# Kernel tuning notes

Hardware: AMD Instinct MI355X
Metric: run time of the kernel (lower is better)

The kernel has to match this reference:

```python
import jax, jax.numpy as jnp
import numpy as np

S, N, H = 4096, 32, 512

def setup_inputs() -> dict:
    key = jax.random.key(0)
    ks = jax.random.split(key, 8)
    scale = 1.0 / np.sqrt(H)
    return {
        "hidden": jax.random.normal(ks[0], (N, H), dtype=jnp.float32),
        "encoder_outputs": jax.random.normal(ks[1], (S, N, H), dtype=jnp.float32),
        "W_w": jax.random.uniform(ks[2], (H, H), jnp.float32, -scale, scale),
        "W_b": jax.random.uniform(ks[3], (H,), jnp.float32, -scale, scale),
        "U_w": jax.random.uniform(ks[4], (H, H), jnp.float32, -scale, scale),
        "U_b": jax.random.uniform(ks[5], (H,), jnp.float32, -scale, scale),
        "v_w": jax.random.uniform(ks[6], (1, H), jnp.float32, -scale, scale),
        "v_b": jax.random.uniform(ks[7], (1,), jnp.float32, -scale, scale),
    }

def reference(hidden, encoder_outputs, W_w, W_b, U_w, U_b, v_w, v_b):
    # W(hidden): [N,H] -> broadcast over seq dim (equivalent to expand then Linear)
    wh = hidden @ W_w.T + W_b                      # [N, H]
    ue = jnp.einsum('snh,kh->snk', encoder_outputs, U_w) + U_b  # [S, N, H]
    energy = jnp.tanh(wh[None, :, :] + ue)         # [S, N, H]
    score = jnp.einsum('snh,oh->sno', energy, v_w) + v_b        # [S, N, 1]
    attention_weights = jax.nn.softmax(score, axis=0)           # softmax over seq
    context = jnp.sum(attention_weights * encoder_outputs, axis=0)  # [N, H]
    return (context, attention_weights)
```

## Files before the change

kernel.cpp:

```cpp
#include <hip/hip_runtime.h>
#include <hip/hip_bf16.h>

#define Sdim 4096
#define Ndim 32
#define Hdim 512
#define Mdim (Sdim * 32)

typedef __bf16 bf16x8 __attribute__((ext_vector_type(8)));
typedef float f32x4 __attribute__((ext_vector_type(4)));

__device__ __forceinline__ void load_lds16(const void* g, void* l) {
    __builtin_amdgcn_global_load_lds(
        (const __attribute__((address_space(1))) void*)g,
        (__attribute__((address_space(3))) void*)l, 16, 0, 0);
}

__device__ __forceinline__ float ftanh(float x) {
    float e = __expf(2.f * x);
    return 1.f - 2.f / (e + 1.f);
}

__global__ __launch_bounds__(256) void k_prep_bias(
    const float* __restrict__ hidden, const float* __restrict__ Ww,
    const float* __restrict__ Wb, const float* __restrict__ Ubias,
    float* __restrict__ bias_t) {
    const int t = threadIdx.x, w = t >> 6, lane = t & 63;
    const int cc = blockIdx.x * 4 + w;
    const float4 w0 = *(const float4*)(Ww + (size_t)cc * Hdim + lane * 8);
    const float4 w1 = *(const float4*)(Ww + (size_t)cc * Hdim + lane * 8 + 4);
    const float wb = Wb[cc] + Ubias[cc];
    for (int n = 0; n < Ndim; ++n) {
        const float4 h0 = *(const float4*)(hidden + n * Hdim + lane * 8);
        const float4 h1 = *(const float4*)(hidden + n * Hdim + lane * 8 + 4);
        float p = w0.x * h0.x + w0.y * h0.y + w0.z * h0.z + w0.w * h0.w +
                  w1.x * h1.x + w1.y * h1.y + w1.z * h1.z + w1.w * h1.w;
        p += __shfl_xor(p, 1);  p += __shfl_xor(p, 2);
        p += __shfl_xor(p, 4);  p += __shfl_xor(p, 8);
        p += __shfl_xor(p, 16); p += __shfl_xor(p, 32);
        if (lane == 0) bias_t[cc * Ndim + n] = p + wb;
    }
}

__global__ __launch_bounds__(256) void k_cvt(
    const float* __restrict__ src, unsigned short* __restrict__ dst) {
    const int i = blockIdx.x * 256 + threadIdx.x;
    float4 v = ((const float4*)src)[i];
    union { __hip_bfloat162 h[2]; ushort4 u; } r;
    r.h[0] = __float22bfloat162_rn(make_float2(v.x, v.y));
    r.h[1] = __float22bfloat162_rn(make_float2(v.z, v.w));
    ((ushort4*)dst)[i] = r.u;
}

__global__ __launch_bounds__(256, 3) void k_gemm_score(
    const float* __restrict__ enc,
    const unsigned short* __restrict__ Ub,
    const float* __restrict__ bias_t,
    const float* __restrict__ vw,
    float* __restrict__ scorep) {
    __shared__ __align__(16) unsigned short Asm[64 * 72];
    __shared__ __align__(16) unsigned short Bsm[256 * 64];
    __shared__ float ssm[4][64];

    const int t = threadIdx.x;
    const int lane = t & 63;
    const int w = t >> 6;
    const int c = lane & 15;
    const int q = lane >> 4;

    const int rowblk = blockIdx.x >> 1;
    const int colblk = blockIdx.x & 1;
    const int mBase = rowblk * 64;
    const int colBase = colblk * 256;

    const int ar = t >> 2;
    const int aq = t & 3;
    const float* aptr = enc + (size_t)(mBase + ar) * Hdim + aq * 16;
    unsigned short* awr = &Asm[ar * 72 + aq * 16];

    const int brow = lane >> 3;
    const int gchunk = (lane & 7) ^ (brow & 7);
    const unsigned short* bptr[8];
    unsigned short* bdst[8];
#pragma unroll
    for (int j = 0; j < 8; ++j) {
        const int r0 = w * 64 + j * 8;
        bptr[j] = Ub + (size_t)(colBase + r0 + brow) * Hdim + gchunk * 8;
        bdst[j] = &Bsm[r0 * 64];
    }

    f32x4 acc[4][4];
#pragma unroll
    for (int i = 0; i < 4; ++i)
#pragma unroll
        for (int j = 0; j < 4; ++j) acc[i][j] = (f32x4){0.f, 0.f, 0.f, 0.f};

    float4 pa0 = *(const float4*)(aptr + 0);
    float4 pa1 = *(const float4*)(aptr + 4);
    float4 pa2 = *(const float4*)(aptr + 8);
    float4 pa3 = *(const float4*)(aptr + 12);

#pragma unroll
    for (int kk = 0; kk < 8; ++kk) {
        __syncthreads();
        union { __hip_bfloat162 h[4]; bf16x8 v; } p0, p1;
        p0.h[0] = __float22bfloat162_rn(make_float2(pa0.x, pa0.y));
        p0.h[1] = __float22bfloat162_rn(make_float2(pa0.z, pa0.w));
        p0.h[2] = __float22bfloat162_rn(make_float2(pa1.x, pa1.y));
        p0.h[3] = __float22bfloat162_rn(make_float2(pa1.z, pa1.w));
        p1.h[0] = __float22bfloat162_rn(make_float2(pa2.x, pa2.y));
        p1.h[1] = __float22bfloat162_rn(make_float2(pa2.z, pa2.w));
        p1.h[2] = __float22bfloat162_rn(make_float2(pa3.x, pa3.y));
        p1.h[3] = __float22bfloat162_rn(make_float2(pa3.z, pa3.w));
        *(bf16x8*)(awr) = p0.v;
        *(bf16x8*)(awr + 8) = p1.v;
#pragma unroll
        for (int j = 0; j < 8; ++j)
            load_lds16(bptr[j] + kk * 64, bdst[j]);
        __syncthreads();
        if (kk < 7) {
            pa0 = *(const float4*)(aptr + (kk + 1) * 64);
            pa1 = *(const float4*)(aptr + (kk + 1) * 64 + 4);
            pa2 = *(const float4*)(aptr + (kk + 1) * 64 + 8);
            pa3 = *(const float4*)(aptr + (kk + 1) * 64 + 12);
        }
#pragma unroll
        for (int kh = 0; kh < 2; ++kh) {
            bf16x8 af[4], bfr[4];
#pragma unroll
            for (int mi = 0; mi < 4; ++mi)
                af[mi] = *(const bf16x8*)&Asm[(mi * 16 + c) * 72 + kh * 32 + q * 8];
#pragma unroll
            for (int ni = 0; ni < 4; ++ni) {
                const int r = w * 64 + ni * 16 + c;
                const int slot = (kh * 4 + q) ^ (c & 7);
                bfr[ni] = *(const bf16x8*)&Bsm[r * 64 + slot * 8];
            }
#pragma unroll
            for (int mi = 0; mi < 4; ++mi)
#pragma unroll
                for (int ni = 0; ni < 4; ++ni)
                    acc[mi][ni] = __builtin_amdgcn_mfma_f32_16x16x32_bf16(
                        af[mi], bfr[ni], acc[mi][ni], 0, 0, 0);
        }
    }

    float vcol[4];
#pragma unroll
    for (int ni = 0; ni < 4; ++ni)
        vcol[ni] = vw[colBase + w * 64 + ni * 16 + c];

#pragma unroll
    for (int mi = 0; mi < 4; ++mi) {
#pragma unroll
        for (int reg = 0; reg < 4; ++reg) {
            const int rl = mi * 16 + q * 4 + reg;
            const int n = rl & 31;
            float p = 0.f;
#pragma unroll
            for (int ni = 0; ni < 4; ++ni) {
                const int col = colBase + w * 64 + ni * 16 + c;
                float e = acc[mi][ni][reg] + bias_t[col * Ndim + n];
                p += vcol[ni] * ftanh(e);
            }
            p += __shfl_xor(p, 1);
            p += __shfl_xor(p, 2);
            p += __shfl_xor(p, 4);
            p += __shfl_xor(p, 8);
            if (c == 0) ssm[w][rl] = p;
        }
    }
    __syncthreads();
    if (t < 64) {
        const int m = mBase + t;
        const float s = ssm[0][t] + ssm[1][t] + ssm[2][t] + ssm[3][t];
        scorep[colblk * Mdim + (m & 31) * Sdim + (m >> 5)] = s;
    }
}

__global__ __launch_bounds__(256) void k_softmax(
    const float* __restrict__ scorep,
    float* __restrict__ wts) {
    const int n = blockIdx.x;
    const int t = threadIdx.x;
    const int w = t >> 6;
    __shared__ float row[Sdim];
    __shared__ float red[8];
    const float4* s0 = (const float4*)(scorep + n * Sdim);
    const float4* s1 = (const float4*)(scorep + Mdim + n * Sdim);

    float mx = -1e30f;
    for (int i = t; i < Sdim / 4; i += 256) {
        float4 a = s0[i], b = s1[i];
        float4 v;
        v.x = a.x + b.x; v.y = a.y + b.y; v.z = a.z + b.z; v.w = a.w + b.w;
        ((float4*)row)[i] = v;
        mx = fmaxf(mx, fmaxf(fmaxf(v.x, v.y), fmaxf(v.z, v.w)));
    }
#pragma unroll
    for (int o = 32; o > 0; o >>= 1) mx = fmaxf(mx, __shfl_xor(mx, o));
    if ((t & 63) == 0) red[w] = mx;
    __syncthreads();
    mx = fmaxf(fmaxf(red[0], red[1]), fmaxf(red[2], red[3]));

    float sum = 0.f;
    for (int i = t; i < Sdim; i += 256) sum += __expf(row[i] - mx);
#pragma unroll
    for (int o = 32; o > 0; o >>= 1) sum += __shfl_xor(sum, o);
    if ((t & 63) == 0) red[4 + w] = sum;
    __syncthreads();
    sum = red[4] + red[5] + red[6] + red[7];
    const float inv = 1.f / sum;
    for (int i = t; i < Sdim; i += 256)
        wts[n * Sdim + i] = __expf(row[i] - mx) * inv;
}

__global__ __launch_bounds__(256) void k_transpose(
    const float* __restrict__ wts, float* __restrict__ out_w) {
    __shared__ float tl[Ndim][129];
    const int s0 = blockIdx.x * 128;
    const int t = threadIdx.x;
    const int rr = t >> 3, cb = (t & 7) * 4;
#pragma unroll
    for (int j = 0; j < 4; ++j)
        *(float4*)&tl[rr][cb + j * 32] =
            *(const float4*)(wts + (size_t)rr * Sdim + s0 + cb + j * 32);
    __syncthreads();
    const int sl = t >> 1, nb = (t & 1) * 16;
#pragma unroll
    for (int j = 0; j < 4; ++j) {
        const int n0 = nb + j * 4;
        float4 v;
        v.x = tl[n0][sl]; v.y = tl[n0 + 1][sl];
        v.z = tl[n0 + 2][sl]; v.w = tl[n0 + 3][sl];
        *(float4*)(out_w + (size_t)(s0 + sl) * Ndim + n0) = v;
    }
}

__global__ __launch_bounds__(256) void k_context(
    const float* __restrict__ enc, const float* __restrict__ wts,
    float* __restrict__ part) {
    const int n = blockIdx.x & 31;
    const int sc = blockIdx.x >> 5;
    const int s0 = sc * 128;
    const int t = threadIdx.x;
    const int hv = t & 127;
    const int sl = t >> 7;
    const float* wrow = wts + (size_t)n * Sdim + s0;
    float4 a0 = {0, 0, 0, 0}, a1 = {0, 0, 0, 0};
    float4 a2 = {0, 0, 0, 0}, a3 = {0, 0, 0, 0};
    for (int i = sl * 4; i < 128; i += 8) {
        const float w0 = wrow[i], w1 = wrow[i + 1];
        const float w2 = wrow[i + 2], w3 = wrow[i + 3];
        const float4 e0 = *(const float4*)(enc + ((size_t)(s0 + i) * Ndim + n) * Hdim + hv * 4);
        const float4 e1 = *(const float4*)(enc + ((size_t)(s0 + i + 1) * Ndim + n) * Hdim + hv * 4);
        const float4 e2 = *(const float4*)(enc + ((size_t)(s0 + i + 2) * Ndim + n) * Hdim + hv * 4);
        const float4 e3 = *(const float4*)(enc + ((size_t)(s0 + i + 3) * Ndim + n) * Hdim + hv * 4);
        a0.x += w0 * e0.x; a0.y += w0 * e0.y; a0.z += w0 * e0.z; a0.w += w0 * e0.w;
        a1.x += w1 * e1.x; a1.y += w1 * e1.y; a1.z += w1 * e1.z; a1.w += w1 * e1.w;
        a2.x += w2 * e2.x; a2.y += w2 * e2.y; a2.z += w2 * e2.z; a2.w += w2 * e2.w;
        a3.x += w3 * e3.x; a3.y += w3 * e3.y; a3.z += w3 * e3.z; a3.w += w3 * e3.w;
    }
    a0.x += a1.x + a2.x + a3.x; a0.y += a1.y + a2.y + a3.y;
    a0.z += a1.z + a2.z + a3.z; a0.w += a1.w + a2.w + a3.w;
    __shared__ float4 red[128];
    if (sl == 1) red[hv] = a0;
    __syncthreads();
    if (sl == 0) {
        const float4 b = red[hv];
        float4 r;
        r.x = a0.x + b.x; r.y = a0.y + b.y; r.z = a0.z + b.z; r.w = a0.w + b.w;
        *(float4*)(part + (size_t)(sc * 32 + n) * Hdim + hv * 4) = r;
    }
}

__global__ __launch_bounds__(256) void k_ctx_reduce(
    const float* __restrict__ part, float* __restrict__ out) {
    const int j = blockIdx.x * 256 + threadIdx.x;
    float4 s = {0, 0, 0, 0};
    for (int i = 0; i < 32; ++i) {
        const float4 v = ((const float4*)part)[i * 4096 + j];
        s.x += v.x; s.y += v.y; s.z += v.z; s.w += v.w;
    }
    ((float4*)out)[j] = s;
}

extern "C" void kernel_launch(void* const* d_in, const int* in_sizes, int n_in,
                              void* d_out, int out_size, void* d_ws,
                              size_t ws_size, hipStream_t stream) {
    const float* hidden = (const float*)d_in[0];
    const float* enc    = (const float*)d_in[1];
    const float* Ww     = (const float*)d_in[2];
    const float* Wb     = (const float*)d_in[3];
    const float* Uw     = (const float*)d_in[4];
    const float* Ubias  = (const float*)d_in[5];
    const float* vw     = (const float*)d_in[6];

    float* out = (float*)d_out;

    char* ws = (char*)d_ws;
    float* wts           = (float*)(ws);
    unsigned short* Ub16 = (unsigned short*)(ws + (512 << 10));
    float* scorep        = (float*)(ws + (1024 << 10));
    float* bias_t        = (float*)(ws + (2048 << 10));
    float* part          = (float*)(ws + (512 << 10));

    k_prep_bias<<<128, 256, 0, stream>>>(hidden, Ww, Wb, Ubias, bias_t);
    k_cvt<<<256, 256, 0, stream>>>(Uw, Ub16);
    k_gemm_score<<<(Mdim / 64) * 2, 256, 0, stream>>>(enc, Ub16, bias_t, vw,
                                                      scorep);
    k_softmax<<<Ndim, 256, 0, stream>>>(scorep, wts);
    k_transpose<<<Sdim / 128, 256, 0, stream>>>(wts, out + Ndim * Hdim);
    k_context<<<Ndim * (Sdim / 128), 256, 0, stream>>>(enc, wts, part);
    k_ctx_reduce<<<16, 256, 0, stream>>>(part, out);
}
```

Measured before the change: 593.6 us.

## Pre-convert encoder outputs to bf16 and use 128x256 tile GEMM with async LDS loads

Adds a separate pass that converts the fp32 encoder outputs to bf16 in workspace. The score GEMM then uses direct global-to-LDS loads for both operands and a larger 128-row tile with 512 threads, so each block reuses the U tile across more rows. The extra pass writes 128 MB and reads 256 MB, and the GEMM then rereads the 128 MB bf16 copy, adding traffic in exchange for simpler GEMM loads and better reuse. A fallback to the old kernel is kept for when the workspace is too small.

Result: slower. 655.0 us (+10.4%).

```diff
diff --git a/kernel.cpp b/kernel.cpp
--- a/kernel.cpp
+++ b/kernel.cpp
@@ -8,6 +8,7 @@
 
 typedef __bf16 bf16x8 __attribute__((ext_vector_type(8)));
 typedef float f32x4 __attribute__((ext_vector_type(4)));
+typedef unsigned short ushort8v __attribute__((ext_vector_type(8)));
 
 __device__ __forceinline__ void load_lds16(const void* g, void* l) {
     __builtin_amdgcn_global_load_lds(
@@ -51,32 +52,147 @@
     ((ushort4*)dst)[i] = r.u;
 }
 
-__global__ __launch_bounds__(256, 3) void k_gemm_score(
-    const float* __restrict__ enc,
+__global__ __launch_bounds__(256) void k_cvt_enc(
+    const float* __restrict__ src, unsigned short* __restrict__ dst) {
+    const size_t i = (size_t)blockIdx.x * 256 + threadIdx.x;
+    const float4 a = ((const float4*)src)[2 * i];
+    const float4 b = ((const float4*)src)[2 * i + 1];
+    union { __hip_bfloat162 h[4]; ushort8v v; } r;
+    r.h[0] = __float22bfloat162_rn(make_float2(a.x, a.y));
+    r.h[1] = __float22bfloat162_rn(make_float2(a.z, a.w));
+    r.h[2] = __float22bfloat162_rn(make_float2(b.x, b.y));
+    r.h[3] = __float22bfloat162_rn(make_float2(b.z, b.w));
+    ((ushort8v*)dst)[i] = r.v;
+}
+
+__global__ __launch_bounds__(512, 3) void k_gemm_score(
+    const unsigned short* __restrict__ encb,
     const unsigned short* __restrict__ Ub,
     const float* __restrict__ bias_t,
     const float* __restrict__ vw,
     float* __restrict__ scorep) {
+    __shared__ __align__(16) unsigned short Asm[128 * 64];
+    __shared__ __align__(16) unsigned short Bsm[256 * 64];
+    __shared__ float ssm[4][128];
+
+    const int t = threadIdx.x;
+    const int lane = t & 63;
+    const int w = t >> 6;
+    const int wM = w >> 2;
+    const int wN = w & 3;
+    const int c = lane & 15;
+    const int q = lane >> 4;
+
+    const int rowblk = blockIdx.x >> 1;
+    const int colblk = blockIdx.x & 1;
+    const int mBase = rowblk * 128;
+    const int colBase = colblk * 256;
+
+    const int l3 = lane >> 3;
+    const int gch = (lane & 7) ^ (l3 & 7);
+    const unsigned short* aSrc[2];
+    unsigned short* aDst[2];
+#pragma unroll
+    for (int i = 0; i < 2; ++i) {
+        const int j = 2 * w + i;
+        aSrc[i] = encb + (size_t)(mBase + j * 8 + l3) * Hdim + gch * 8;
+        aDst[i] = &Asm[j * 8 * 64];
+    }
+    const unsigned short* bSrc[4];
+    unsigned short* bDst[4];
+#pragma unroll
+    for (int i = 0; i < 4; ++i) {
+        const int j = 4 * w + i;
+        bSrc[i] = Ub + (size_t)(colBase + j * 8 + l3) * Hdim + gch * 8;
+        bDst[i] = &Bsm[j * 8 * 64];
+    }
+
+    f32x4 acc[4][4];
+#pragma unroll
+    for (int i = 0; i < 4; ++i)
+#pragma unroll
+        for (int j = 0; j < 4; ++j) acc[i][j] = (f32x4){0.f, 0.f, 0.f, 0.f};
+
+#pragma unroll
+    for (int kk = 0; kk < 8; ++kk) {
+        __syncthreads();
+        load_lds16(aSrc[0] + kk * 64, aDst[0]);
+        load_lds16(aSrc[1] + kk * 64, aDst[1]);
+#pragma unroll
+        for (int i = 0; i < 4; ++i)
+            load_lds16(bSrc[i] + kk * 64, bDst[i]);
+        __syncthreads();
+
+#pragma unroll
+        for (int kh = 0; kh < 2; ++kh) {
+            bf16x8 af[4], bfr[4];
+            const int slot = (kh * 4 + q) ^ (c & 7);
+#pragma unroll
+            for (int mi = 0; mi < 4; ++mi) {
+                const int r = wM * 64 + mi * 16 + c;
+                af[mi] = *(const bf16x8*)&Asm[r * 64 + slot * 8];
+            }
+#pragma unroll
+            for (int ni = 0; ni < 4; ++ni) {
+                const int r = wN * 64 + ni * 16 + c;
+                bfr[ni] = *(const bf16x8*)&Bsm[r * 64 + slot * 8];
+            }
+#pragma unroll
+            for (int mi = 0; mi < 4; ++mi)
+#pragma unroll
+                for (int ni = 0; ni < 4; ++ni)
+                    acc[mi][ni] = __builtin_amdgcn_mfma_f32_16x16x32_bf16(
+                        af[mi], bfr[ni], acc[mi][ni], 0, 0, 0);
+        }
+    }
+
+    float vcol[4];
+#pragma unroll
+    for (int ni = 0; ni < 4; ++ni)
+        vcol[ni] = vw[colBase + wN * 64 + ni * 16 + c];
+
+#pragma unroll
+    for (int mi = 0; mi < 4; ++mi) {
+#pragma unroll
+        for (int reg = 0; reg < 4; ++reg) {
+            const int rl = wM * 64 + mi * 16 + q * 4 + reg;
+            const int n = rl & 31;
+            float p = 0.f;
+#pragma unroll
+            for (int ni = 0; ni < 4; ++ni) {
+                const int col = colBase + wN * 64 + ni * 16 + c;
+                float e = acc[mi][ni][reg] + bias_t[col * Ndim + n];
+                p += vcol[ni] * ftanh(e);
+            }
+            p += __shfl_xor(p, 1);
+            p += __shfl_xor(p, 2);
+            p += __shfl_xor(p, 4);
+            p += __shfl_xor(p, 8);
+            if (c == 0) ssm[wN][rl] = p;
+        }
+    }
+    __syncthreads();
+    if (t < 128) {
+        const int m = mBase + t;
+        const float s = ssm[0][t] + ssm[1][t] + ssm[2][t] + ssm[3][t];
+        scorep[colblk * Mdim + (m & 31) * Sdim + (m >> 5)] = s;
+    }
+}
+
+__global__ __launch_bounds__(256, 3) void k_gemm_score_fb(
+    const float* __restrict__ enc, const unsigned short* __restrict__ Ub,
+    const float* __restrict__ bias_t, const float* __restrict__ vw,
+    float* __restrict__ scorep) {
     __shared__ __align__(16) unsigned short Asm[64 * 72];
     __shared__ __align__(16) unsigned short Bsm[256 * 64];
     __shared__ float ssm[4][64];
-
-    const int t = threadIdx.x;
-    const int lane = t & 63;
-    const int w = t >> 6;
-    const int c = lane & 15;
-    const int q = lane >> 4;
-
-    const int rowblk = blockIdx.x >> 1;
-    const int colblk = blockIdx.x & 1;
-    const int mBase = rowblk * 64;
-    const int colBase = colblk * 256;
-
-    const int ar = t >> 2;
-    const int aq = t & 3;
+    const int t = threadIdx.x, lane = t & 63, w = t >> 6;
+    const int c = lane & 15, q = lane >> 4;
+    const int rowblk = blockIdx.x >> 1, colblk = blockIdx.x & 1;
+    const int mBase = rowblk * 64, colBase = colblk * 256;
+    const int ar = t >> 2, aq = t & 3;
     const float* aptr = enc + (size_t)(mBase + ar) * Hdim + aq * 16;
     unsigned short* awr = &Asm[ar * 72 + aq * 16];
-
     const int brow = lane >> 3;
     const int gchunk = (lane & 7) ^ (brow & 7);
     const unsigned short* bptr[8];
@@ -87,18 +203,13 @@
         bptr[j] = Ub + (size_t)(colBase + r0 + brow) * Hdim + gchunk * 8;
         bdst[j] = &Bsm[r0 * 64];
     }
-
     f32x4 acc[4][4];
 #pragma unroll
     for (int i = 0; i < 4; ++i)
 #pragma unroll
         for (int j = 0; j < 4; ++j) acc[i][j] = (f32x4){0.f, 0.f, 0.f, 0.f};
-
-    float4 pa0 = *(const float4*)(aptr + 0);
-    float4 pa1 = *(const float4*)(aptr + 4);
-    float4 pa2 = *(const float4*)(aptr + 8);
-    float4 pa3 = *(const float4*)(aptr + 12);
-
+    float4 pa0 = *(const float4*)(aptr + 0), pa1 = *(const float4*)(aptr + 4);
+    float4 pa2 = *(const float4*)(aptr + 8), pa3 = *(const float4*)(aptr + 12);
 #pragma unroll
     for (int kk = 0; kk < 8; ++kk) {
         __syncthreads();
@@ -114,8 +225,7 @@
         *(bf16x8*)(awr) = p0.v;
         *(bf16x8*)(awr + 8) = p1.v;
 #pragma unroll
-        for (int j = 0; j < 8; ++j)
-            load_lds16(bptr[j] + kk * 64, bdst[j]);
+        for (int j = 0; j < 8; ++j) load_lds16(bptr[j] + kk * 64, bdst[j]);
         __syncthreads();
         if (kk < 7) {
             pa0 = *(const float4*)(aptr + (kk + 1) * 64);
@@ -143,12 +253,9 @@
                         af[mi], bfr[ni], acc[mi][ni], 0, 0, 0);
         }
     }
-
     float vcol[4];
 #pragma unroll
-    for (int ni = 0; ni < 4; ++ni)
-        vcol[ni] = vw[colBase + w * 64 + ni * 16 + c];
-
+    for (int ni = 0; ni < 4; ++ni) vcol[ni] = vw[colBase + w * 64 + ni * 16 + c];
 #pragma unroll
     for (int mi = 0; mi < 4; ++mi) {
 #pragma unroll
@@ -178,8 +285,7 @@
 }
 
 __global__ __launch_bounds__(256) void k_softmax(
-    const float* __restrict__ scorep,
-    float* __restrict__ wts) {
+    const float* __restrict__ scorep, float* __restrict__ wts) {
     const int n = blockIdx.x;
     const int t = threadIdx.x;
     const int w = t >> 6;
@@ -187,7 +293,6 @@
     __shared__ float red[8];
     const float4* s0 = (const float4*)(scorep + n * Sdim);
     const float4* s1 = (const float4*)(scorep + Mdim + n * Sdim);
-
     float mx = -1e30f;
     for (int i = t; i < Sdim / 4; i += 256) {
         float4 a = s0[i], b = s1[i];
@@ -201,7 +306,6 @@
     if ((t & 63) == 0) red[w] = mx;
     __syncthreads();
     mx = fmaxf(fmaxf(red[0], red[1]), fmaxf(red[2], red[3]));
-
     float sum = 0.f;
     for (int i = t; i < Sdim; i += 256) sum += __expf(row[i] - mx);
 #pragma unroll
@@ -298,16 +402,24 @@
     float* out = (float*)d_out;
 
     char* ws = (char*)d_ws;
-    float* wts           = (float*)(ws);
-    unsigned short* Ub16 = (unsigned short*)(ws + (512 << 10));
-    float* scorep        = (float*)(ws + (1024 << 10));
-    float* bias_t        = (float*)(ws + (2048 << 10));
-    float* part          = (float*)(ws + (512 << 10));
+    unsigned short* Ub16 = (unsigned short*)(ws);
+    float* bias_t        = (float*)(ws + (512 << 10));
+    float* scorep        = (float*)(ws + (576 << 10));
+    float* wts           = (float*)(ws + (1600 << 10));
+    float* part          = (float*)(ws + (2112 << 10));
+    unsigned short* encb = (unsigned short*)(ws + (8 << 20));
+    const size_t REQ = (8ull << 20) + (size_t)Mdim * Hdim * 2;
 
     k_prep_bias<<<128, 256, 0, stream>>>(hidden, Ww, Wb, Ubias, bias_t);
     k_cvt<<<256, 256, 0, stream>>>(Uw, Ub16);
-    k_gemm_score<<<(Mdim / 64) * 2, 256, 0, stream>>>(enc, Ub16, bias_t, vw,
-                                                      scorep);
+    if (ws_size >= REQ) {
+        k_cvt_enc<<<32768, 256, 0, stream>>>(enc, encb);
+        k_gemm_score<<<(Mdim / 128) * 2, 512, 0, stream>>>(encb, Ub16, bias_t,
+                                                           vw, scorep);
+    } else {
+        k_gemm_score_fb<<<(Mdim / 64) * 2, 256, 0, stream>>>(enc, Ub16, bias_t,
+                                                             vw, scorep);
+    }
     k_softmax<<<Ndim, 256, 0, stream>>>(scorep, wts);
     k_transpose<<<Sdim / 128, 256, 0, stream>>>(wts, out + Ndim * Hdim);
     k_context<<<Ndim * (Sdim / 128), 256, 0, stream>>>(enc, wts, part);
```

## Pre-convert encoder to bf16 and keep U strip resident in LDS for GEMM

Applied to the files above, without the earlier changes.

A separate kernel now converts encoder_outputs to bf16 once. The score GEMM is restructured into persistent 512-thread blocks: each block holds a full 128-column strip of U in 128KB of dynamic LDS and loops over four row tiles, loading A fragments straight from global memory into registers with register double-buffering. The bias prep and U conversion kernels are merged into one launch, and the transpose kernel is folded into softmax as strided stores, which also now sums four partial scores. This aims to cut redundant fp32 encoder reads and per-tile LDS staging of U, at the cost of an extra full conversion pass over the encoder and uncoalesced weight-output writes.

Result: slower. 650.0 us (+9.5%).

```diff
diff --git a/kernel.cpp b/kernel.cpp
--- a/kernel.cpp
+++ b/kernel.cpp
@@ -8,6 +8,7 @@
 
 typedef __bf16 bf16x8 __attribute__((ext_vector_type(8)));
 typedef float f32x4 __attribute__((ext_vector_type(4)));
+typedef unsigned short ushort8v __attribute__((ext_vector_type(8)));
 
 __device__ __forceinline__ void load_lds16(const void* g, void* l) {
     __builtin_amdgcn_global_load_lds(
@@ -20,166 +21,175 @@
     return 1.f - 2.f / (e + 1.f);
 }
 
-__global__ __launch_bounds__(256) void k_prep_bias(
+__global__ __launch_bounds__(256) void k_prep(
     const float* __restrict__ hidden, const float* __restrict__ Ww,
     const float* __restrict__ Wb, const float* __restrict__ Ubias,
-    float* __restrict__ bias_t) {
-    const int t = threadIdx.x, w = t >> 6, lane = t & 63;
-    const int cc = blockIdx.x * 4 + w;
-    const float4 w0 = *(const float4*)(Ww + (size_t)cc * Hdim + lane * 8);
-    const float4 w1 = *(const float4*)(Ww + (size_t)cc * Hdim + lane * 8 + 4);
-    const float wb = Wb[cc] + Ubias[cc];
-    for (int n = 0; n < Ndim; ++n) {
-        const float4 h0 = *(const float4*)(hidden + n * Hdim + lane * 8);
-        const float4 h1 = *(const float4*)(hidden + n * Hdim + lane * 8 + 4);
-        float p = w0.x * h0.x + w0.y * h0.y + w0.z * h0.z + w0.w * h0.w +
-                  w1.x * h1.x + w1.y * h1.y + w1.z * h1.z + w1.w * h1.w;
-        p += __shfl_xor(p, 1);  p += __shfl_xor(p, 2);
-        p += __shfl_xor(p, 4);  p += __shfl_xor(p, 8);
-        p += __shfl_xor(p, 16); p += __shfl_xor(p, 32);
-        if (lane == 0) bias_t[cc * Ndim + n] = p + wb;
-    }
-}
-
-__global__ __launch_bounds__(256) void k_cvt(
+    const float* __restrict__ Uw, float* __restrict__ bias_t,
+    unsigned short* __restrict__ Ub16) {
+    if (blockIdx.x < 128) {
+        const int t = threadIdx.x, w = t >> 6, lane = t & 63;
+        const int cc = blockIdx.x * 4 + w;
+        const float4 w0 = *(const float4*)(Ww + (size_t)cc * Hdim + lane * 8);
+        const float4 w1 = *(const float4*)(Ww + (size_t)cc * Hdim + lane * 8 + 4);
+        const float wb = Wb[cc] + Ubias[cc];
+        for (int n = 0; n < Ndim; ++n) {
+            const float4 h0 = *(const float4*)(hidden + n * Hdim + lane * 8);
+            const float4 h1 = *(const float4*)(hidden + n * Hdim + lane * 8 + 4);
+            float p = w0.x * h0.x + w0.y * h0.y + w0.z * h0.z + w0.w * h0.w +
+                      w1.x * h1.x + w1.y * h1.y + w1.z * h1.z + w1.w * h1.w;
+            p += __shfl_xor(p, 1);  p += __shfl_xor(p, 2);
+            p += __shfl_xor(p, 4);  p += __shfl_xor(p, 8);
+            p += __shfl_xor(p, 16); p += __shfl_xor(p, 32);
+            if (lane == 0) bias_t[cc * Ndim + n] = p + wb;
+        }
+    } else {
+        const int i = (blockIdx.x - 128) * 256 + threadIdx.x;
+        float4 v = ((const float4*)Uw)[i];
+        union { __hip_bfloat162 h[2]; ushort4 u; } r;
+        r.h[0] = __float22bfloat162_rn(make_float2(v.x, v.y));
+        r.h[1] = __float22bfloat162_rn(make_float2(v.z, v.w));
+        ((ushort4*)Ub16)[i] = r.u;
+    }
+}
+
+__global__ __launch_bounds__(256) void k_cvt_enc(
     const float* __restrict__ src, unsigned short* __restrict__ dst) {
-    const int i = blockIdx.x * 256 + threadIdx.x;
-    float4 v = ((const float4*)src)[i];
-    union { __hip_bfloat162 h[2]; ushort4 u; } r;
-    r.h[0] = __float22bfloat162_rn(make_float2(v.x, v.y));
-    r.h[1] = __float22bfloat162_rn(make_float2(v.z, v.w));
-    ((ushort4*)dst)[i] = r.u;
-}
-
-__global__ __launch_bounds__(256, 3) void k_gemm_score(
-    const float* __restrict__ enc,
+    const size_t i = (size_t)blockIdx.x * 256 + threadIdx.x;
+    const float4 a = ((const float4*)src)[2 * i];
+    const float4 b = ((const float4*)src)[2 * i + 1];
+    union { __hip_bfloat162 h[4]; ushort8v v; } r;
+    r.h[0] = __float22bfloat162_rn(make_float2(a.x, a.y));
+    r.h[1] = __float22bfloat162_rn(make_float2(a.z, a.w));
+    r.h[2] = __float22bfloat162_rn(make_float2(b.x, b.y));
+    r.h[3] = __float22bfloat162_rn(make_float2(b.z, b.w));
+    ((ushort8v*)dst)[i] = r.v;
+}
+
+__global__ __launch_bounds__(512, 2) void k_gemm_score(
+    const unsigned short* __restrict__ encb,
     const unsigned short* __restrict__ Ub,
     const float* __restrict__ bias_t,
     const float* __restrict__ vw,
     float* __restrict__ scorep) {
-    __shared__ __align__(16) unsigned short Asm[64 * 72];
-    __shared__ __align__(16) unsigned short Bsm[256 * 64];
-    __shared__ float ssm[4][64];
+    extern __shared__ __align__(16) unsigned short Bsm[];
+    __shared__ float ssm[2][256];
 
     const int t = threadIdx.x;
     const int lane = t & 63;
     const int w = t >> 6;
+    const int wM = w >> 1;
+    const int wN = w & 1;
     const int c = lane & 15;
     const int q = lane >> 4;
 
-    const int rowblk = blockIdx.x >> 1;
-    const int colblk = blockIdx.x & 1;
-    const int mBase = rowblk * 64;
-    const int colBase = colblk * 256;
-
-    const int ar = t >> 2;
-    const int aq = t & 3;
-    const float* aptr = enc + (size_t)(mBase + ar) * Hdim + aq * 16;
-    unsigned short* awr = &Asm[ar * 72 + aq * 16];
-
-    const int brow = lane >> 3;
-    const int gchunk = (lane & 7) ^ (brow & 7);
-    const unsigned short* bptr[8];
-    unsigned short* bdst[8];
-#pragma unroll
-    for (int j = 0; j < 8; ++j) {
-        const int r0 = w * 64 + j * 8;
-        bptr[j] = Ub + (size_t)(colBase + r0 + brow) * Hdim + gchunk * 8;
-        bdst[j] = &Bsm[r0 * 64];
-    }
-
-    f32x4 acc[4][4];
-#pragma unroll
-    for (int i = 0; i < 4; ++i)
-#pragma unroll
-        for (int j = 0; j < 4; ++j) acc[i][j] = (f32x4){0.f, 0.f, 0.f, 0.f};
-
-    float4 pa0 = *(const float4*)(aptr + 0);
-    float4 pa1 = *(const float4*)(aptr + 4);
-    float4 pa2 = *(const float4*)(aptr + 8);
-    float4 pa3 = *(const float4*)(aptr + 12);
-
-#pragma unroll
-    for (int kk = 0; kk < 8; ++kk) {
+    const int strip = blockIdx.x & 3;
+    const int bgroup = blockIdx.x >> 2;
+    const int colBase = strip * 128;
+
+#pragma unroll
+    for (int j = 0; j < 16; ++j) {
+        const int col = w * 16 + j;
+        const unsigned short* src =
+            Ub + (size_t)(colBase + col) * Hdim + (lane ^ (col & 7)) * 8;
+        load_lds16(src, &Bsm[col * Hdim]);
+    }
+
+    float vcol[4];
+#pragma unroll
+    for (int ni = 0; ni < 4; ++ni)
+        vcol[ni] = vw[colBase + wN * 64 + ni * 16 + c];
+
+    __syncthreads();
+
+    for (int p = 0; p < 4; ++p) {
+        const int rowBase = (bgroup + p * 128) * 256;
+        const unsigned short* aRow[4];
+#pragma unroll
+        for (int mi = 0; mi < 4; ++mi)
+            aRow[mi] =
+                encb + (size_t)(rowBase + wM * 64 + mi * 16 + c) * Hdim + q * 8;
+
+        f32x4 acc[4][4];
+#pragma unroll
+        for (int i = 0; i < 4; ++i)
+#pragma unroll
+            for (int j = 0; j < 4; ++j) acc[i][j] = (f32x4){0.f, 0.f, 0.f, 0.f};
+
+        bf16x8 aC[4][2];
+#pragma unroll
+        for (int mi = 0; mi < 4; ++mi)
+#pragma unroll
+            for (int kh = 0; kh < 2; ++kh)
+                aC[mi][kh] = *(const bf16x8*)(aRow[mi] + kh * 32);
+
+#pragma unroll
+        for (int kk = 0; kk < 8; ++kk) {
+            bf16x8 aN[4][2];
+            if (kk < 7) {
+#pragma unroll
+                for (int mi = 0; mi < 4; ++mi)
+#pragma unroll
+                    for (int kh = 0; kh < 2; ++kh)
+                        aN[mi][kh] = *(const bf16x8*)(aRow[mi] +
+                                                      (kk + 1) * 64 + kh * 32);
+            }
+#pragma unroll
+            for (int kh = 0; kh < 2; ++kh) {
+                bf16x8 bfr[4];
+#pragma unroll
+                for (int ni = 0; ni < 4; ++ni) {
+                    const int col = wN * 64 + ni * 16 + c;
+                    const int slot = kk * 8 + ((kh * 4 + q) ^ (col & 7));
+                    bfr[ni] = *(const bf16x8*)&Bsm[col * Hdim + slot * 8];
+                }
+#pragma unroll
+                for (int mi = 0; mi < 4; ++mi)
+#pragma unroll
+                    for (int ni = 0; ni < 4; ++ni)
+                        acc[mi][ni] = __builtin_amdgcn_mfma_f32_16x16x32_bf16(
+                            aC[mi][kh], bfr[ni], acc[mi][ni], 0, 0, 0);
+            }
+            if (kk < 7) {
+#pragma unroll
+                for (int mi = 0; mi < 4; ++mi)
+#pragma unroll
+                    for (int kh = 0; kh < 2; ++kh) aC[mi][kh] = aN[mi][kh];
+            }
+        }
+
+#pragma unroll
+        for (int mi = 0; mi < 4; ++mi) {
+#pragma unroll
+            for (int reg = 0; reg < 4; ++reg) {
+                const int rl = wM * 64 + mi * 16 + q * 4 + reg;
+                const int n = rl & 31;
+                float psum = 0.f;
+#pragma unroll
+                for (int ni = 0; ni < 4; ++ni) {
+                    const int gcol = colBase + wN * 64 + ni * 16 + c;
+                    float e = acc[mi][ni][reg] + bias_t[gcol * Ndim + n];
+                    psum += vcol[ni] * ftanh(e);
+                }
+                psum += __shfl_xor(psum, 1);
+                psum += __shfl_xor(psum, 2);
+                psum += __shfl_xor(psum, 4);
+                psum += __shfl_xor(psum, 8);
+                if (c == 0) ssm[wN][rl] = psum;
+            }
+        }
         __syncthreads();
-        union { __hip_bfloat162 h[4]; bf16x8 v; } p0, p1;
-        p0.h[0] = __float22bfloat162_rn(make_float2(pa0.x, pa0.y));
-        p0.h[1] = __float22bfloat162_rn(make_float2(pa0.z, pa0.w));
-        p0.h[2] = __float22bfloat162_rn(make_float2(pa1.x, pa1.y));
-        p0.h[3] = __float22bfloat162_rn(make_float2(pa1.z, pa1.w));
-        p1.h[0] = __float22bfloat162_rn(make_float2(pa2.x, pa2.y));
-        p1.h[1] = __float22bfloat162_rn(make_float2(pa2.z, pa2.w));
-        p1.h[2] = __float22bfloat162_rn(make_float2(pa3.x, pa3.y));
-        p1.h[3] = __float22bfloat162_rn(make_float2(pa3.z, pa3.w));
-        *(bf16x8*)(awr) = p0.v;
-        *(bf16x8*)(awr + 8) = p1.v;
-#pragma unroll
-        for (int j = 0; j < 8; ++j)
-            load_lds16(bptr[j] + kk * 64, bdst[j]);
+        if (t < 256) {
+            const int m = rowBase + t;
+            scorep[strip * Mdim + (m & 31) * Sdim + (m >> 5)] =
+                ssm[0][t] + ssm[1][t];
+        }
         __syncthreads();
-        if (kk < 7) {
-            pa0 = *(const float4*)(aptr + (kk + 1) * 64);
-            pa1 = *(const float4*)(aptr + (kk + 1) * 64 + 4);
-            pa2 = *(const float4*)(aptr + (kk + 1) * 64 + 8);
-            pa3 = *(const float4*)(aptr + (kk + 1) * 64 + 12);
-        }
-#pragma unroll
-        for (int kh = 0; kh < 2; ++kh) {
-            bf16x8 af[4], bfr[4];
-#pragma unroll
-            for (int mi = 0; mi < 4; ++mi)
-                af[mi] = *(const bf16x8*)&Asm[(mi * 16 + c) * 72 + kh * 32 + q * 8];
-#pragma unroll
-            for (int ni = 0; ni < 4; ++ni) {
-                const int r = w * 64 + ni * 16 + c;
-                const int slot = (kh * 4 + q) ^ (c & 7);
-                bfr[ni] = *(const bf16x8*)&Bsm[r * 64 + slot * 8];
-            }
-#pragma unroll
-            for (int mi = 0; mi < 4; ++mi)
-#pragma unroll
-                for (int ni = 0; ni < 4; ++ni)
-                    acc[mi][ni] = __builtin_amdgcn_mfma_f32_16x16x32_bf16(
-                        af[mi], bfr[ni], acc[mi][ni], 0, 0, 0);
-        }
-    }
-
-    float vcol[4];
-#pragma unroll
-    for (int ni = 0; ni < 4; ++ni)
-        vcol[ni] = vw[colBase + w * 64 + ni * 16 + c];
-
-#pragma unroll
-    for (int mi = 0; mi < 4; ++mi) {
-#pragma unroll
-        for (int reg = 0; reg < 4; ++reg) {
-            const int rl = mi * 16 + q * 4 + reg;
-            const int n = rl & 31;
-            float p = 0.f;
-#pragma unroll
-            for (int ni = 0; ni < 4; ++ni) {
-                const int col = colBase + w * 64 + ni * 16 + c;
-                float e = acc[mi][ni][reg] + bias_t[col * Ndim + n];
-                p += vcol[ni] * ftanh(e);
-            }
-            p += __shfl_xor(p, 1);
-            p += __shfl_xor(p, 2);
-            p += __shfl_xor(p, 4);
-            p += __shfl_xor(p, 8);
-            if (c == 0) ssm[w][rl] = p;
-        }
-    }
-    __syncthreads();
-    if (t < 64) {
-        const int m = mBase + t;
-        const float s = ssm[0][t] + ssm[1][t] + ssm[2][t] + ssm[3][t];
-        scorep[colblk * Mdim + (m & 31) * Sdim + (m >> 5)] = s;
     }
 }
 
 __global__ __launch_bounds__(256) void k_softmax(
-    const float* __restrict__ scorep,
-    float* __restrict__ wts) {
+    const float* __restrict__ scorep, float* __restrict__ wts,
+    float* __restrict__ out_w) {
     const int n = blockIdx.x;
     const int t = threadIdx.x;
     const int w = t >> 6;
@@ -187,12 +197,14 @@
     __shared__ float red[8];
     const float4* s0 = (const float4*)(scorep + n * Sdim);
     const float4* s1 = (const float4*)(scorep + Mdim + n * Sdim);
-
+    const float4* s2 = (const float4*)(scorep + 2 * Mdim + n * Sdim);
+    const float4* s3 = (const float4*)(scorep + 3 * Mdim + n * Sdim);
     float mx = -1e30f;
     for (int i = t; i < Sdim / 4; i += 256) {
-        float4 a = s0[i], b = s1[i];
+        float4 a = s0[i], b = s1[i], cc = s2[i], d = s3[i];
         float4 v;
-        v.x = a.x + b.x; v.y = a.y + b.y; v.z = a.z + b.z; v.w = a.w + b.w;
+        v.x = a.x + b.x + cc.x + d.x; v.y = a.y + b.y + cc.y + d.y;
+        v.z = a.z + b.z + cc.z + d.z; v.w = a.w + b.w + cc.w + d.w;
         ((float4*)row)[i] = v;
         mx = fmaxf(mx, fmaxf(fmaxf(v.x, v.y), fmaxf(v.z, v.w)));
     }
@@ -201,7 +213,6 @@
     if ((t & 63) == 0) red[w] = mx;
     __syncthreads();
     mx = fmaxf(fmaxf(red[0], red[1]), fmaxf(red[2], red[3]));
-
     float sum = 0.f;
     for (int i = t; i < Sdim; i += 256) sum += __expf(row[i] - mx);
 #pragma unroll
@@ -210,29 +221,10 @@
     __syncthreads();
     sum = red[4] + red[5] + red[6] + red[7];
     const float inv = 1.f / sum;
-    for (int i = t; i < Sdim; i += 256)
-        wts[n * Sdim + i] = __expf(row[i] - mx) * inv;
-}
-
-__global__ __launch_bounds__(256) void k_transpose(
-    const float* __restrict__ wts, float* __restrict__ out_w) {
-    __shared__ float tl[Ndim][129];
-    const int s0 = blockIdx.x * 128;
-    const int t = threadIdx.x;
-    const int rr = t >> 3, cb = (t & 7) * 4;
-#pragma unroll
-    for (int j = 0; j < 4; ++j)
-        *(float4*)&tl[rr][cb + j * 32] =
-            *(const float4*)(wts + (size_t)rr * Sdim + s0 + cb + j * 32);
-    __syncthreads();
-    const int sl = t >> 1, nb = (t & 1) * 16;
-#pragma unroll
-    for (int j = 0; j < 4; ++j) {
-        const int n0 = nb + j * 4;
-        float4 v;
-        v.x = tl[n0][sl]; v.y = tl[n0 + 1][sl];
-        v.z = tl[n0 + 2][sl]; v.w = tl[n0 + 3][sl];
-        *(float4*)(out_w + (size_t)(s0 + sl) * Ndim + n0) = v;
+    for (int i = t; i < Sdim; i += 256) {
+        const float wv = __expf(row[i] - mx) * inv;
+        wts[n * Sdim + i] = wv;
+        out_w[(size_t)i * Ndim + n] = wv;
     }
 }
 
@@ -298,18 +290,21 @@
     float* out = (float*)d_out;
 
     char* ws = (char*)d_ws;
-    float* wts           = (float*)(ws);
-    unsigned short* Ub16 = (unsigned short*)(ws + (512 << 10));
-    float* scorep        = (float*)(ws + (1024 << 10));
-    float* bias_t        = (float*)(ws + (2048 << 10));
-    float* part          = (float*)(ws + (512 << 10));
-
-    k_prep_bias<<<128, 256, 0, stream>>>(hidden, Ww, Wb, Ubias, bias_t);
-    k_cvt<<<256, 256, 0, stream>>>(Uw, Ub16);
-    k_gemm_score<<<(Mdim / 64) * 2, 256, 0, stream>>>(enc, Ub16, bias_t, vw,
-                                                      scorep);
-    k_softmax<<<Ndim, 256, 0, stream>>>(scorep, wts);
-    k_transpose<<<Sdim / 128, 256, 0, stream>>>(wts, out + Ndim * Hdim);
+    unsigned short* Ub16 = (unsigned short*)(ws);
+    float* bias_t        = (float*)(ws + (512 << 10));
+    float* scorep        = (float*)(ws + (576 << 10));
+    float* wts           = (float*)(ws + (2624 << 10));
+    float* part          = (float*)(ws + (3136 << 10));
+    unsigned short* encb = (unsigned short*)(ws + (8 << 20));
+
+    (void)hipFuncSetAttribute((const void*)k_gemm_score,
+                              hipFuncAttributeMaxDynamicSharedMemorySize,
+                              131072);
+
+    k_prep<<<384, 256, 0, stream>>>(hidden, Ww, Wb, Ubias, Uw, bias_t, Ub16);
+    k_cvt_enc<<<32768, 256, 0, stream>>>(enc, encb);
+    k_gemm_score<<<512, 512, 131072, stream>>>(encb, Ub16, bias_t, vw, scorep);
+    k_softmax<<<Ndim, 256, 0, stream>>>(scorep, wts, out + Ndim * Hdim);
     k_context<<<Ndim * (Sdim / 128), 256, 0, stream>>>(enc, wts, part);
     k_ctx_reduce<<<16, 256, 0, stream>>>(part, out);
 }
```
